# Kernel tuning notes

Hardware: AMD Instinct MI355X
Metric: run time of the kernel (lower is better)

## Reference

```python
import jax, jax.numpy as jnp
import numpy as np
import math

IN_FEATURES = 729   # n^2 with n = 27 = 3^3
HIDDEN = 2916
OUT_FEATURES = 729
BASE = 3
FACTOR = 0
B, D = 64, 768      # batch, channel dim (x: [B, D, IN_FEATURES])


def _butterfly_factor_to_matrix(twiddle, factor_index):
    # twiddle: (n//b, b, b) -> dense n x n butterfly factor matrix (numpy, setup-time only)
    n_div_b, b, _ = twiddle.shape
    n = b * n_div_b
    stride = b ** factor_index
    # eye(n) rearranged: 'bs (diagblk j stride)' -> (bs, diagblk, j, stride)
    x = np.eye(n, dtype=np.float32).reshape(n, n // (b * stride), b, stride)
    # twiddle rearranged: '(diagblk stride) i j' -> (diagblk, stride, i, j)
    t = twiddle.reshape(n // (b * stride), stride, b, b)
    out = np.einsum('dsij,bdjs->bdis', t, x).reshape(n, n)
    return out.T


def _sparse_mask():
    b = BASE
    log_b_n = int(math.log(math.sqrt(IN_FEATURES), b))
    n = b ** log_b_n
    twiddle = np.arange(1, n * b + 1, dtype=np.float32).reshape(n // b, b, b)
    m1 = _butterfly_factor_to_matrix(twiddle, FACTOR)
    mask = np.kron(m1, m1)
    return jnp.asarray((mask > 0).astype(np.float32))  # [729, 729] 0/1 mask


def setup_inputs() -> dict:
    key = jax.random.key(0)
    k1, k2, k3, k4 = jax.random.split(key, 4)
    x = jax.random.normal(k1, (B, D, IN_FEATURES), jnp.float32)
    w1 = jax.random.normal(k2, (HIDDEN, IN_FEATURES), jnp.float32) / math.sqrt(IN_FEATURES)
    w2 = jax.random.normal(k3, (OUT_FEATURES, HIDDEN), jnp.float32) / math.sqrt(HIDDEN)
    b2 = jax.random.normal(k4, (OUT_FEATURES,), jnp.float32) * 0.01
    return {"x": x, "w1": w1, "w2": w2, "b2": b2, "sparse_mask": _sparse_mask()}


def reference(x, w1, w2, b2, sparse_mask):
    # attn_s[s,t] = sum_d fc1.W[d,s] * fc2.W[t,d], then butterfly-masked
    attn = jnp.einsum('ds,td->st', w1, w2) * sparse_mask  # [in, out]
    out = jnp.einsum('bds,st->bdt', x, attn) + b2          # [B, D, out]
    return jax.nn.gelu(out, approximate=False)             # torch nn.GELU uses exact erf
```

## Files before the change

kernel.cpp:

```cpp
#include <hip/hip_runtime.h>
#include <hip/hip_bf16.h>


__device__ __forceinline__ float gelu_f(float v) {
    float u2 = v * v;
    float z = -1.5957691216f * v * fmaf(0.044715f, u2, 1.0f);
    float e = __expf(z);
    return v / (1.0f + e);
}

__global__ __launch_bounds__(512) void bfly_attn_kernel(
        const float* __restrict__ w1,
        const float* __restrict__ w2,
        float* __restrict__ attn)
{
    const int g  = blockIdx.x;
    const int G1 = g / 9, G2 = g % 9;
    const int tid = threadIdx.x;

    int idx[9];
    #pragma unroll
    for (int i = 0; i < 3; ++i)
        #pragma unroll
        for (int j = 0; j < 3; ++j)
            idx[3*i + j] = 81*G1 + 27*i + 3*G2 + j;

    float acc[81];
    #pragma unroll
    for (int k = 0; k < 81; ++k) acc[k] = 0.0f;

    for (int d = tid; d < 2916; d += 512) {
        float a[9], b[9];
        #pragma unroll
        for (int k = 0; k < 9; ++k) {
            a[k] = w1[d * 729 + idx[k]];
            b[k] = w2[idx[k] * 2916 + d];
        }
        #pragma unroll
        for (int ls = 0; ls < 9; ++ls)
            #pragma unroll
            for (int lt = 0; lt < 9; ++lt)
                acc[ls*9 + lt] = fmaf(a[ls], b[lt], acc[ls*9 + lt]);
    }

    __shared__ float red[8][81];
    const int lane = tid & 63, wave = tid >> 6;
    #pragma unroll
    for (int k = 0; k < 81; ++k) {
        float v = acc[k];
        #pragma unroll
        for (int off = 32; off > 0; off >>= 1)
            v += __shfl_down(v, off, 64);
        if (lane == 0) red[wave][k] = v;
    }
    __syncthreads();
    if (tid < 81) {
        float s = 0.0f;
        #pragma unroll
        for (int w = 0; w < 8; ++w) s += red[w][tid];
        attn[g * 81 + tid] = s;
    }
}

#define ROWS 16

__global__ __launch_bounds__(256) void bfly_mlp_kernel(
        const float* __restrict__ xg,
        const float* __restrict__ attn,
        const float* __restrict__ b2g,
        float* __restrict__ outg)
{
    __shared__ float xs[ROWS * 729];

    const int tid = threadIdx.x;
    const long long rowbase = (long long)blockIdx.x * ROWS;

    {
        const uint4* src = (const uint4*)(xg + rowbase * 729);
        uint4* dst = (uint4*)xs;
        for (int i = tid; i < (ROWS * 729) / 4; i += 256) dst[i] = src[i];
    }
    __syncthreads();

    if (tid < 243) {
        const int t1 = tid / 9;
        const int G2 = tid % 9;
        const int G1 = t1 / 3;
        const int li = t1 % 3;
        const int tb = 27 * t1 + 3 * G2;
        const int sb = 81 * G1 + 3 * G2;
        const int g  = 9 * G1 + G2;

        float a[9][3];
        #pragma unroll
        for (int ls = 0; ls < 9; ++ls)
            #pragma unroll
            for (int j = 0; j < 3; ++j)
                a[ls][j] = attn[g * 81 + ls * 9 + 3 * li + j];

        float bias[3];
        #pragma unroll
        for (int j = 0; j < 3; ++j) bias[j] = b2g[tb + j];

        for (int r = 0; r < ROWS; ++r) {
            const int xb = r * 729 + sb;
            float xv[9];
            #pragma unroll
            for (int i2 = 0; i2 < 3; ++i2)
                #pragma unroll
                for (int j2 = 0; j2 < 3; ++j2)
                    xv[3*i2 + j2] = xs[xb + 27*i2 + j2];

            float acc0 = bias[0], acc1 = bias[1], acc2 = bias[2];
            #pragma unroll
            for (int ls = 0; ls < 9; ++ls) {
                acc0 = fmaf(xv[ls], a[ls][0], acc0);
                acc1 = fmaf(xv[ls], a[ls][1], acc1);
                acc2 = fmaf(xv[ls], a[ls][2], acc2);
            }

            const long long ob = (rowbase + r) * 729 + tb;
            outg[ob + 0] = gelu_f(acc0);
            outg[ob + 1] = gelu_f(acc1);
            outg[ob + 2] = gelu_f(acc2);
        }
    }
}

extern "C" void kernel_launch(void* const* d_in, const int* in_sizes, int n_in,
                              void* d_out, int out_size, void* d_ws, size_t ws_size,
                              hipStream_t stream) {
    const float* x  = (const float*)d_in[0];
    const float* w1 = (const float*)d_in[1];
    const float* w2 = (const float*)d_in[2];
    const float* b2 = (const float*)d_in[3];

    float* attn = (float*)d_ws;

    bfly_attn_kernel<<<81, 512, 0, stream>>>(w1, w2, attn);

    const int n_rows = 64 * 768;
    bfly_mlp_kernel<<<n_rows / ROWS, 256, 0, stream>>>(
        x, attn, b2, (float*)d_out);
}
```

Before: 319.5 us.

## Split attn reduction over d-chunks with shared staging and atomics; shrink MLP tile

The attention-weight kernel is restructured so that 243 blocks each stage a 108-wide chunk of d for one G1 group into shared memory. Partial sums are accumulated with atomicAdd into a buffer zeroed by a new kernel, replacing 81 blocks that used strided global loads and a shuffle reduction. The MLP kernel halves rows per block to 8, hoists the attn and bias loads above the x staging, and adds unroll 2. GELU's division becomes a hardware reciprocal. The changes add an extra launch and float atomics, which make summation order nondeterministic.

```diff
diff --git a/kernel.cpp b/kernel.cpp
--- a/kernel.cpp
+++ b/kernel.cpp
@@ -6,63 +6,67 @@
     float u2 = v * v;
     float z = -1.5957691216f * v * fmaf(0.044715f, u2, 1.0f);
     float e = __expf(z);
-    return v / (1.0f + e);
+    return v * __builtin_amdgcn_rcpf(1.0f + e);
 }
 
-__global__ __launch_bounds__(512) void bfly_attn_kernel(
+__global__ void attn_zero_kernel(float* __restrict__ attn) {
+    int i = blockIdx.x * 256 + threadIdx.x;
+    if (i < 81 * 81) attn[i] = 0.0f;
+}
+
+#define CH 108
+
+__global__ __launch_bounds__(256) void bfly_attn_kernel(
         const float* __restrict__ w1,
         const float* __restrict__ w2,
         float* __restrict__ attn)
 {
-    const int g  = blockIdx.x;
-    const int G1 = g / 9, G2 = g % 9;
-    const int tid = threadIdx.x;
+    const int G1    = blockIdx.x % 9;
+    const int d0    = (blockIdx.x / 9) * CH;
+    const int tid   = threadIdx.x;
 
-    int idx[9];
-    #pragma unroll
-    for (int i = 0; i < 3; ++i)
-        #pragma unroll
-        for (int j = 0; j < 3; ++j)
-            idx[3*i + j] = 81*G1 + 27*i + 3*G2 + j;
+    __shared__ float ws1[CH * 81];
+    __shared__ float ws2[81 * CH];
 
-    float acc[81];
-    #pragma unroll
-    for (int k = 0; k < 81; ++k) acc[k] = 0.0f;
-
-    for (int d = tid; d < 2916; d += 512) {
-        float a[9], b[9];
-        #pragma unroll
-        for (int k = 0; k < 9; ++k) {
-            a[k] = w1[d * 729 + idx[k]];
-            b[k] = w2[idx[k] * 2916 + d];
-        }
-        #pragma unroll
-        for (int ls = 0; ls < 9; ++ls)
-            #pragma unroll
-            for (int lt = 0; lt < 9; ++lt)
-                acc[ls*9 + lt] = fmaf(a[ls], b[lt], acc[ls*9 + lt]);
+    for (int i = tid; i < CH * 81; i += 256) {
+        int dl = i / 81, c = i % 81;
+        ws1[i] = w1[(d0 + dl) * 729 + 81 * G1 + c];
     }
-
-    __shared__ float red[8][81];
-    const int lane = tid & 63, wave = tid >> 6;
-    #pragma unroll
-    for (int k = 0; k < 81; ++k) {
-        float v = acc[k];
-        #pragma unroll
-        for (int off = 32; off > 0; off >>= 1)
-            v += __shfl_down(v, off, 64);
-        if (lane == 0) red[wave][k] = v;
+    for (int i = tid; i < 81 * CH; i += 256) {
+        int tl = i / CH, dl = i % CH;
+        ws2[i] = w2[(81 * G1 + tl) * 2916 + d0 + dl];
     }
     __syncthreads();
-    if (tid < 81) {
-        float s = 0.0f;
+
+    if (tid < 243) {
+        const int G2  = tid / 27;
+        const int ls  = (tid % 27) / 3;
+        const int lt0 = (tid % 3) * 3;
+        const int s_l = 27 * (ls / 3) + 3 * G2 + (ls % 3);
+        int t_l[3];
         #pragma unroll
-        for (int w = 0; w < 8; ++w) s += red[w][tid];
-        attn[g * 81 + tid] = s;
+        for (int j = 0; j < 3; ++j) {
+            int lt = lt0 + j;
+            t_l[j] = 27 * (lt / 3) + 3 * G2 + (lt % 3);
+        }
+
+        float a0 = 0.f, a1 = 0.f, a2 = 0.f;
+        for (int dl = 0; dl < CH; ++dl) {
+            float av = ws1[dl * 81 + s_l];
+            a0 = fmaf(av, ws2[t_l[0] * CH + dl], a0);
+            a1 = fmaf(av, ws2[t_l[1] * CH + dl], a1);
+            a2 = fmaf(av, ws2[t_l[2] * CH + dl], a2);
+        }
+
+        const int g = 9 * G1 + G2;
+        float* dst = &attn[g * 81 + ls * 9 + lt0];
+        atomicAdd(dst + 0, a0);
+        atomicAdd(dst + 1, a1);
+        atomicAdd(dst + 2, a2);
     }
 }
 
-#define ROWS 16
+#define ROWS 8
 
 __global__ __launch_bounds__(256) void bfly_mlp_kernel(
         const float* __restrict__ xg,
@@ -75,6 +79,26 @@
     const int tid = threadIdx.x;
     const long long rowbase = (long long)blockIdx.x * ROWS;
 
+    float a[9][3], bias[3];
+    int tb = 0, sb = 0;
+    const bool active = (tid < 243);
+    if (active) {
+        const int t1 = tid / 9;
+        const int G2 = tid % 9;
+        const int G1 = t1 / 3;
+        const int li = t1 % 3;
+        tb = 27 * t1 + 3 * G2;
+        sb = 81 * G1 + 3 * G2;
+        const int g  = 9 * G1 + G2;
+        #pragma unroll
+        for (int ls = 0; ls < 9; ++ls)
+            #pragma unroll
+            for (int j = 0; j < 3; ++j)
+                a[ls][j] = attn[g * 81 + ls * 9 + 3 * li + j];
+        #pragma unroll
+        for (int j = 0; j < 3; ++j) bias[j] = b2g[tb + j];
+    }
+
     {
         const uint4* src = (const uint4*)(xg + rowbase * 729);
         uint4* dst = (uint4*)xs;
@@ -82,26 +106,8 @@
     }
     __syncthreads();
 
-    if (tid < 243) {
-        const int t1 = tid / 9;
-        const int G2 = tid % 9;
-        const int G1 = t1 / 3;
-        const int li = t1 % 3;
-        const int tb = 27 * t1 + 3 * G2;
-        const int sb = 81 * G1 + 3 * G2;
-        const int g  = 9 * G1 + G2;
-
-        float a[9][3];
-        #pragma unroll
-        for (int ls = 0; ls < 9; ++ls)
-            #pragma unroll
-            for (int j = 0; j < 3; ++j)
-                a[ls][j] = attn[g * 81 + ls * 9 + 3 * li + j];
-
-        float bias[3];
-        #pragma unroll
-        for (int j = 0; j < 3; ++j) bias[j] = b2g[tb + j];
-
+    if (active) {
+        #pragma unroll 2
         for (int r = 0; r < ROWS; ++r) {
             const int xb = r * 729 + sb;
             float xv[9];
@@ -137,7 +143,8 @@
 
     float* attn = (float*)d_ws;
 
-    bfly_attn_kernel<<<81, 512, 0, stream>>>(w1, w2, attn);
+    attn_zero_kernel<<<26, 256, 0, stream>>>(attn);
+    bfly_attn_kernel<<<9 * 27, 256, 0, stream>>>(w1, w2, attn);
 
     const int n_rows = 64 * 768;
     bfly_mlp_kernel<<<n_rows / ROWS, 256, 0, stream>>>(
```

Result: faster. 281.5 us (-11.9%).
